# Performance work log

Hardware: AMD Instinct MI355X
Metric: run time of the kernel (lower is better)

## Reference

```python
import jax, jax.numpy as jnp
import numpy as np

VOXEL_SIZE = 0.4
GAMMA = 1.1  # VoxelPointsSampler.GAMMA
PC_MIN, PC_MAX = -75.2, 75.2


def setup_inputs() -> dict:
    key = jax.random.key(0)
    ks = jax.random.split(key, 6)
    N, M, C, S = 200000, 256, 5, 128
    xy = jax.random.uniform(ks[0], (N, 2), minval=PC_MIN, maxval=PC_MAX)
    z = jax.random.uniform(ks[1], (N, 1), minval=-2.0, maxval=4.0)
    feat = jax.random.normal(ks[2], (N, C - 3))
    points = jnp.concatenate([xy, z, feat], axis=1)  # [N, 5]
    ctr = jax.random.uniform(ks[3], (M, 2), minval=PC_MIN * 0.9, maxval=PC_MAX * 0.9)
    cz = jnp.zeros((M, 1), jnp.float32)
    dims = jax.random.uniform(ks[4], (M, 3), minval=1.0, maxval=5.0)
    yaw = jax.random.uniform(ks[5], (M, 1), minval=-3.14, maxval=3.14)
    boxes = jnp.concatenate([ctr, cz, dims, yaw], axis=1)  # [M, 7]
    pc_start = jnp.array([PC_MIN, PC_MIN], dtype=jnp.float32)
    return {"points": points, "boxes": boxes, "pc_start": pc_start, "num_sample": S}


def reference(points, boxes, pc_start, num_sample):
    N, C = points.shape
    M = boxes.shape[0]
    # --- voxel-level radius ball query (distances in voxel units) ---
    pcoords = (points[:, :2] - pc_start) / VOXEL_SIZE          # [N, 2]
    qcoords = (boxes[:, :2] - pc_start) / VOXEL_SIZE           # [M, 2]
    r_vox = jnp.linalg.norm(boxes[:, 3:5] * 0.5, axis=-1) * GAMMA / VOXEL_SIZE  # [M]
    dist = jnp.linalg.norm(qcoords[:, None, :] - pcoords[None, :, :], axis=-1)  # [M, N]
    vmask = (dist < r_vox[:, None]).any(axis=0)                # [N]
    # --- cylindrical pool (metric space); invalid points pushed out of every radius ---
    BIG = jnp.asarray(1e6, points.dtype)
    xy_m = jnp.where(vmask[:, None], points[:, :2], BIG)       # [N, 2]
    radii = jnp.linalg.norm(boxes[:, 3:5] * 0.5, axis=-1) * GAMMA  # [M]
    dis = jnp.linalg.norm(boxes[:, None, :2] - xy_m[None, :, :], axis=-1)  # [M, N]
    pmask = (dis <= radii[:, None]).astype(points.dtype)       # 0/1 [M, N]
    sm, sidx = jax.lax.top_k(pmask, num_sample)                # [M, S]
    smb = sm > 0.5                                             # bool [M, S]
    # unique indices across all sampled slots (fixed-size for jit)
    uniq, inv = jnp.unique(sidx.ravel(), return_inverse=True,
                           size=M * num_sample, fill_value=0)
    query_points = points[uniq]                                # [M*S, C] (padded)
    sampled_points = points[sidx] * smb[:, :, None]            # [M, S, C]
    idx = inv.reshape(M, num_sample).astype(jnp.int32) * smb   # [M, S]
    return sampled_points, idx, query_points
```

## Files before the change

### kernel.cpp

```cpp
#include <hip/hip_runtime.h>

typedef unsigned long long u64;
typedef unsigned int u32;
typedef unsigned short u16;
typedef unsigned char u8;

#define VOX 0.4f
#define GAM 1.1f
#define NCX 16
#define CELLW 32.0f
#define CAP 64

__device__ __forceinline__ float dist2d(float ax, float ay, float bx, float by) {
  float dx = __fsub_rn(ax, bx);
  float dy = __fsub_rn(ay, by);
  return __fsqrt_rn(__fadd_rn(__fmul_rn(dx, dx), __fmul_rn(dy, dy)));
}

__device__ __forceinline__ float box_radius(const float* __restrict__ boxes, int m) {
  float hx = __fmul_rn(boxes[m * 7 + 3], 0.5f);
  float hy = __fmul_rn(boxes[m * 7 + 4], 0.5f);
  float nr = __fsqrt_rn(__fadd_rn(__fmul_rn(hx, hx), __fmul_rn(hy, hy)));
  return __fmul_rn(nr, GAM);
}

__device__ __forceinline__ void box_voxel(const float* __restrict__ boxes, int m,
                                          float psx, float psy,
                                          float& qx, float& qy, float& r) {
  qx = __fdiv_rn(__fsub_rn(boxes[m * 7 + 0], psx), VOX);
  qy = __fdiv_rn(__fsub_rn(boxes[m * 7 + 1], psy), VOX);
  float hx = __fmul_rn(boxes[m * 7 + 3], 0.5f);
  float hy = __fmul_rn(boxes[m * 7 + 4], 0.5f);
  float nr = __fsqrt_rn(__fadd_rn(__fmul_rn(hx, hx), __fmul_rn(hy, hy)));
  r = __fdiv_rn(__fmul_rn(nr, GAM), VOX);
}

__global__ void k_prep(const float* __restrict__ boxes, const float* __restrict__ pc_start,
                       float* __restrict__ qxv, float* __restrict__ qyv, float* __restrict__ rv,
                       int* __restrict__ cellCnt, u16* __restrict__ cellList, int M) {
  const int tid = threadIdx.x;
  if (blockIdx.x == 0) {
    for (int m = tid; m < M; m += 256) {
      float qx, qy, r;
      box_voxel(boxes, m, pc_start[0], pc_start[1], qx, qy, r);
      qxv[m] = qx; qyv[m] = qy; rv[m] = r;
    }
    return;
  }
  const int cell = blockIdx.x - 1;
  const int cx = cell & (NCX - 1), cy = cell >> 4;
  const int wv = tid >> 6, lane = tid & 63;
  __shared__ int wcnt[4];
  const float x0 = (cx == 0) ? -3e38f : cx * CELLW;
  const float x1 = (cx == NCX - 1) ? 3e38f : (cx + 1) * CELLW;
  const float y0 = (cy == 0) ? -3e38f : cy * CELLW;
  const float y1 = (cy == NCX - 1) ? 3e38f : (cy + 1) * CELLW;
  bool hit = false;
  if (tid < M) {
    float qx, qy, r;
    box_voxel(boxes, tid, pc_start[0], pc_start[1], qx, qy, r);
    float ddx = fmaxf(0.0f, fmaxf(x0 - qx, qx - x1));
    float ddy = fmaxf(0.0f, fmaxf(y0 - qy, qy - y1));
    float rr = r + 0.01f;
    hit = (ddx * ddx + ddy * ddy <= rr * rr);
  }
  u64 b = __ballot(hit);
  if (lane == 0) wcnt[wv] = __popcll(b);
  __syncthreads();
  int base = 0;
  for (int w = 0; w < wv; ++w) base += wcnt[w];
  if (hit) {
    int slot = base + __popcll(b & ((1ULL << lane) - 1ULL));
    if (slot < CAP) cellList[cell * CAP + slot] = (u16)tid;
  }
  if (tid == 0) cellCnt[cell] = wcnt[0] + wcnt[1] + wcnt[2] + wcnt[3];
}

__global__ void k_vmask_count(const float* __restrict__ pts, const float* __restrict__ boxes,
                              const float* __restrict__ qxv, const float* __restrict__ qyv,
                              const float* __restrict__ rv,
                              const int* __restrict__ cellCnt, const u16* __restrict__ cellList,
                              u64* __restrict__ vbits, u64* __restrict__ pbits,
                              u64* __restrict__ bmG, int* __restrict__ cpng,
                              const float* __restrict__ pc_start,
                              int N, int M) {
  __shared__ float cpx[256], cpy[256];
  __shared__ int cpn[256];
  __shared__ int ccell[256];
  __shared__ float sbx[256], sby[256], sbr[256];
  __shared__ u64 bm[256][4];
  __shared__ int wcnt[4];
  const int tid = threadIdx.x;
  const int blk = blockIdx.x;
  const int n = blk * 256 + tid;
  const int wv = tid >> 6, lane = tid & 63;
  const float psx = pc_start[0], psy = pc_start[1];
  const bool valid = (n < N);

  bm[tid][0] = 0; bm[tid][1] = 0; bm[tid][2] = 0; bm[tid][3] = 0;
  if (tid < 4) pbits[blk * 4 + tid] = 0;
  if (tid < M) {
    sbx[tid] = boxes[tid * 7 + 0];
    sby[tid] = boxes[tid * 7 + 1];
    sbr[tid] = box_radius(boxes, tid);
  }

  float px = 1e6f, py = 1e6f, pvx = 0.f, pvy = 0.f;
  if (valid) {
    px = pts[n * 5 + 0];
    py = pts[n * 5 + 1];
    pvx = __fdiv_rn(__fsub_rn(px, psx), VOX);
    pvy = __fdiv_rn(__fsub_rn(py, psy), VOX);
  }

  bool flag = false;
  int mycell = 0;
  if (valid) {
    int cx = (int)floorf(pvx * (1.0f / CELLW));
    int cy = (int)floorf(pvy * (1.0f / CELLW));
    cx = cx < 0 ? 0 : (cx > NCX - 1 ? NCX - 1 : cx);
    cy = cy < 0 ? 0 : (cy > NCX - 1 ? NCX - 1 : cy);
    mycell = cy * NCX + cx;
    const int k = cellCnt[mycell];
    if (k <= CAP) {
      for (int j = 0; j < k; ++j) {
        const int m = cellList[mycell * CAP + j];
        float d = dist2d(qxv[m], qyv[m], pvx, pvy);
        if (d < rv[m]) { flag = true; break; }
      }
    } else {
      for (int m = 0; m < M; ++m) {
        float d = dist2d(qxv[m], qyv[m], pvx, pvy);
        if (d < rv[m]) { flag = true; break; }
      }
    }
  }
  u64 b = __ballot(flag);
  if (lane == 0) {
    vbits[n >> 6] = b;
    wcnt[wv] = __popcll(b);
  }
  __syncthreads();

  int base = 0;
  for (int w = 0; w < wv; ++w) base += wcnt[w];
  if (flag) {
    int slot = base + __popcll(b & ((1ULL << lane) - 1ULL));
    cpx[slot] = px;
    cpy[slot] = py;
    cpn[slot] = n;
    ccell[slot] = mycell;
  }
  __syncthreads();
  const int nfl = wcnt[0] + wcnt[1] + wcnt[2] + wcnt[3];
  if (tid < nfl) cpng[blk * 256 + tid] = cpn[tid];

  if (tid < nfl) {
    const float mx = cpx[tid], my = cpy[tid];
    const int cell = ccell[tid];
    const int k = cellCnt[cell];
    const u64 bit = 1ULL << (tid & 63);
    const int word = tid >> 6;
    if (k <= CAP) {
      for (int j = 0; j < k; ++j) {
        const int m = cellList[cell * CAP + j];
        float d = dist2d(sbx[m], sby[m], mx, my);
        if (d <= sbr[m]) atomicOr(&bm[m][word], bit);
      }
    } else {
      for (int m = 0; m < M; ++m) {
        float d = dist2d(sbx[m], sby[m], mx, my);
        if (d <= sbr[m]) atomicOr(&bm[m][word], bit);
      }
    }
  }
  __syncthreads();

  if (tid < M) {
    u64* dst = bmG + ((size_t)blk * M + tid) * 4;
    dst[0] = bm[tid][0]; dst[1] = bm[tid][1];
    dst[2] = bm[tid][2]; dst[3] = bm[tid][3];
  }
}

__global__ void __launch_bounds__(1024) k_scanfill(
    const float* __restrict__ pts, const float* __restrict__ boxes,
    const u64* __restrict__ bmG, const int* __restrict__ cpng,
    const u64* __restrict__ vbits, int* __restrict__ kcount,
    int* __restrict__ sidx, u64* __restrict__ pbits,
    int N, int M, int S, int nchunk) {
  const int m = blockIdx.x;
  const int t = threadIdx.x;
  const int lane = t & 63, wv = t >> 6;
  __shared__ int wsum[16];
  __shared__ int zws[16];

  u64 w0 = 0, w1 = 0, w2 = 0, w3 = 0;
  int v = 0;
  if (t < nchunk) {
    const u64* bp = bmG + ((size_t)t * M + m) * 4;
    w0 = bp[0]; w1 = bp[1]; w2 = bp[2]; w3 = bp[3];
    v = __popcll(w0) + __popcll(w1) + __popcll(w2) + __popcll(w3);
  }
  int incl = v;
  for (int d = 1; d < 64; d <<= 1) {
    int x = __shfl_up(incl, d);
    if (lane >= d) incl += x;
  }
  if (lane == 63) wsum[wv] = incl;
  __syncthreads();
  if (t < 16) {
    int s = wsum[t];
    for (int d = 1; d < 16; d <<= 1) {
      int x = __shfl_up(s, d);
      if (t >= d) s += x;
    }
    wsum[t] = s;
  }
  __syncthreads();
  const int wbase = (wv > 0) ? wsum[wv - 1] : 0;
  const int off = wbase + incl - v;
  const int total = wsum[15];
  const int k0 = total < S ? total : S;
  if (t == 0) kcount[m] = k0;

  if (t < nchunk && v > 0 && off < S) {
    const int* pbase = cpng + t * 256;
    int cum = off;
    int curw = -1;
    u64 acc = 0;
    u64 ws4[4] = {w0, w1, w2, w3};
    for (int wi = 0; wi < 4 && cum < S; ++wi) {
      u64 w = ws4[wi];
      while (w && cum < S) {
        int j = (wi << 6) + __builtin_ctzll(w);
        w &= w - 1;
        int pn = pbase[j];
        sidx[m * S + cum] = pn;
        const int wd = pn >> 6;
        if (wd != curw) {
          if (curw >= 0) atomicOr(&pbits[curw], acc);
          curw = wd;
          acc = 0;
        }
        acc |= 1ULL << (pn & 63);
        ++cum;
      }
    }
    if (curw >= 0) atomicOr(&pbits[curw], acc);
  }

  if (k0 >= S) return;
  const float bx = boxes[m * 7 + 0], by = boxes[m * 7 + 1];
  const float r = box_radius(boxes, m);
  const u64 ltmask = (1ULL << lane) - 1ULL;
  int fill = k0;
  for (int p0 = 0; p0 < N && fill < S; p0 += 1024) {
    const int n = p0 + t;
    const bool validn = n < N;
    bool one = false;
    if (validn) {
      u64 wbit = vbits[n >> 6];
      if ((wbit >> (n & 63)) & 1ULL) {
        float d = dist2d(bx, by, pts[n * 5 + 0], pts[n * 5 + 1]);
        one = (d <= r);
      }
    }
    const bool z = validn && !one;
    u64 b = __ballot(z);
    if (lane == 0) zws[wv] = __popcll(b);
    __syncthreads();
    int zbase = 0, ztot = 0;
    for (int ww = 0; ww < 16; ++ww) {
      int c = zws[ww];
      if (ww < wv) zbase += c;
      ztot += c;
    }
    bool setp = false;
    if (z) {
      int pos = fill + zbase + __popcll(b & ltmask);
      if (pos < S) { sidx[m * S + pos] = n; setp = true; }
    }
    u64 setmask = __ballot(setp);
    if (lane == 0 && setmask) atomicOr(&pbits[n >> 6], setmask);
    fill += ztot;
    __syncthreads();
  }
}

__global__ void __launch_bounds__(1024) k_sumscan(const u64* __restrict__ pbits,
                                                  int* __restrict__ boff, int nb) {
  __shared__ int wsum[16];
  const int t = threadIdx.x, lane = t & 63, wv = t >> 6;
  int v = 0;
  if (t < nb) {
    const u64* p = pbits + (size_t)t * 4;
    v = __popcll(p[0]) + __popcll(p[1]) + __popcll(p[2]) + __popcll(p[3]);
  }
  int incl = v;
  for (int d = 1; d < 64; d <<= 1) {
    int x = __shfl_up(incl, d);
    if (lane >= d) incl += x;
  }
  if (lane == 63) wsum[wv] = incl;
  __syncthreads();
  if (t < 16) {
    int s = wsum[t];
    for (int d = 1; d < 16; d <<= 1) {
      int x = __shfl_up(s, d);
      if (t >= d) s += x;
    }
    wsum[t] = s;
  }
  __syncthreads();
  const int base = (wv > 0) ? wsum[wv - 1] : 0;
  if (t < nb) boff[t] = base + incl - v;
  if (t == 0) boff[1024] = wsum[15];
}

__global__ void k_outpad(const float* __restrict__ pts, const int* __restrict__ sidx,
                         const int* __restrict__ kcount, const u64* __restrict__ pbits,
                         const int* __restrict__ boff,
                         float* __restrict__ out_samp, float* __restrict__ out_idx,
                         float* __restrict__ out_query, int MS, int S) {
  const int e = blockIdx.x * 256 + threadIdx.x;
  if (e >= MS) return;
  const int U = boff[1024];
  if (e >= U) {
    float* q = out_query + (size_t)e * 5;
    q[0] = pts[0]; q[1] = pts[1]; q[2] = pts[2]; q[3] = pts[3]; q[4] = pts[4];
  }
  const int m = e / S;
  const int s = e - m * S;
  const int n = sidx[e];
  const int c = n >> 8, w = n >> 6;
  int rank = boff[c];
  for (int k = c * 4; k < w; ++k) rank += __popcll(pbits[k]);
  rank += __popcll(pbits[w] & ((1ULL << (n & 63)) - 1ULL));
  const float* p = pts + (size_t)n * 5;
  float* q = out_query + (size_t)rank * 5;
  q[0] = p[0]; q[1] = p[1]; q[2] = p[2]; q[3] = p[3]; q[4] = p[4];
  float* o = out_samp + (size_t)e * 5;
  if (s < kcount[m]) {
    o[0] = p[0]; o[1] = p[1]; o[2] = p[2]; o[3] = p[3]; o[4] = p[4];
    out_idx[e] = (float)rank;
  } else {
    o[0] = 0.f; o[1] = 0.f; o[2] = 0.f; o[3] = 0.f; o[4] = 0.f;
    out_idx[e] = 0.f;
  }
}

extern "C" void kernel_launch(void* const* d_in, const int* in_sizes, int n_in,
                              void* d_out, int out_size, void* d_ws, size_t ws_size,
                              hipStream_t stream) {
  const float* pts = (const float*)d_in[0];
  const float* boxes = (const float*)d_in[1];
  const float* pc_start = (const float*)d_in[2];
  const int N = in_sizes[0] / 5;
  const int M = in_sizes[1] / 7;
  const int S = out_size / (M * 11);
  const int MS = M * S;

  float* out_samp = (float*)d_out;
  float* out_idx = out_samp + (size_t)MS * 5;
  float* out_query = out_idx + (size_t)MS;

  const int nb = (N + 255) / 256;
  const int nchunk = nb;

  char* w = (char*)d_ws;
  auto take = [&](size_t bytes) {
    char* p = w;
    w += (bytes + 15) & ~(size_t)15;
    return (void*)p;
  };
  u64* vbits     = (u64*)take((size_t)(nb * 4) * 8);
  u64* pbits     = (u64*)take((size_t)(nb * 4) * 8);
  u64* bmG       = (u64*)take((size_t)nchunk * M * 4 * 8);
  int* cpng      = (int*)take((size_t)nchunk * 256 * 4);
  int* sidx      = (int*)take((size_t)MS * 4);
  int* kcount    = (int*)take((size_t)M * 4);
  int* boff      = (int*)take((size_t)1025 * 4);
  float* qxv     = (float*)take((size_t)M * 4);
  float* qyv     = (float*)take((size_t)M * 4);
  float* rv      = (float*)take((size_t)M * 4);
  int* cellCnt   = (int*)take((size_t)NCX * NCX * 4);
  u16* cellList  = (u16*)take((size_t)NCX * NCX * CAP * 2);

  k_prep<<<NCX * NCX + 1, 256, 0, stream>>>(boxes, pc_start, qxv, qyv, rv,
                                            cellCnt, cellList, M);
  k_vmask_count<<<nb, 256, 0, stream>>>(pts, boxes, qxv, qyv, rv, cellCnt, cellList,
                                        vbits, pbits, bmG, cpng, pc_start, N, M);
  k_scanfill<<<M, 1024, 0, stream>>>(pts, boxes, bmG, cpng, vbits, kcount,
                                     sidx, pbits, N, M, S, nchunk);
  k_sumscan<<<1, 1024, 0, stream>>>(pbits, boff, nb);
  k_outpad<<<(MS + 255) / 256, 256, 0, stream>>>(pts, sidx, kcount, pbits, boff,
                                                 out_samp, out_idx, out_query, MS, S);
}
```

Before: 88.89 us.

## Fuse prefix-scan into output kernel and compute box voxel params in shared memory

Removes the single-block scan kernel: every block of the output kernel now recomputes the per-chunk prefix offsets of the selected-point bitmasks in shared memory, and launches with 1024 threads. Box voxel coordinates and radii, previously written to global memory by a dedicated block in the prep kernel, are now computed per block into shared memory inside the vmask kernel, with an added barrier. This saves one kernel launch and its global round trip, at the cost of redundant scan and box work in every block.

```diff
diff --git a/kernel.cpp b/kernel.cpp
--- a/kernel.cpp
+++ b/kernel.cpp
@@ -36,19 +36,10 @@
 }
 
 __global__ void k_prep(const float* __restrict__ boxes, const float* __restrict__ pc_start,
-                       float* __restrict__ qxv, float* __restrict__ qyv, float* __restrict__ rv,
                        int* __restrict__ cellCnt, u16* __restrict__ cellList, int M) {
+  const int cell = blockIdx.x;
+  const int cx = cell & (NCX - 1), cy = cell >> 4;
   const int tid = threadIdx.x;
-  if (blockIdx.x == 0) {
-    for (int m = tid; m < M; m += 256) {
-      float qx, qy, r;
-      box_voxel(boxes, m, pc_start[0], pc_start[1], qx, qy, r);
-      qxv[m] = qx; qyv[m] = qy; rv[m] = r;
-    }
-    return;
-  }
-  const int cell = blockIdx.x - 1;
-  const int cx = cell & (NCX - 1), cy = cell >> 4;
   const int wv = tid >> 6, lane = tid & 63;
   __shared__ int wcnt[4];
   const float x0 = (cx == 0) ? -3e38f : cx * CELLW;
@@ -77,8 +68,6 @@
 }
 
 __global__ void k_vmask_count(const float* __restrict__ pts, const float* __restrict__ boxes,
-                              const float* __restrict__ qxv, const float* __restrict__ qyv,
-                              const float* __restrict__ rv,
                               const int* __restrict__ cellCnt, const u16* __restrict__ cellList,
                               u64* __restrict__ vbits, u64* __restrict__ pbits,
                               u64* __restrict__ bmG, int* __restrict__ cpng,
@@ -88,6 +77,7 @@
   __shared__ int cpn[256];
   __shared__ int ccell[256];
   __shared__ float sbx[256], sby[256], sbr[256];
+  __shared__ float sqx[256], sqy[256], srv[256];
   __shared__ u64 bm[256][4];
   __shared__ int wcnt[4];
   const int tid = threadIdx.x;
@@ -103,6 +93,9 @@
     sbx[tid] = boxes[tid * 7 + 0];
     sby[tid] = boxes[tid * 7 + 1];
     sbr[tid] = box_radius(boxes, tid);
+    float qx, qy, r;
+    box_voxel(boxes, tid, psx, psy, qx, qy, r);
+    sqx[tid] = qx; sqy[tid] = qy; srv[tid] = r;
   }
 
   float px = 1e6f, py = 1e6f, pvx = 0.f, pvy = 0.f;
@@ -112,6 +105,7 @@
     pvx = __fdiv_rn(__fsub_rn(px, psx), VOX);
     pvy = __fdiv_rn(__fsub_rn(py, psy), VOX);
   }
+  __syncthreads();
 
   bool flag = false;
   int mycell = 0;
@@ -125,13 +119,13 @@
     if (k <= CAP) {
       for (int j = 0; j < k; ++j) {
         const int m = cellList[mycell * CAP + j];
-        float d = dist2d(qxv[m], qyv[m], pvx, pvy);
-        if (d < rv[m]) { flag = true; break; }
+        float d = dist2d(sqx[m], sqy[m], pvx, pvy);
+        if (d < srv[m]) { flag = true; break; }
       }
     } else {
       for (int m = 0; m < M; ++m) {
-        float d = dist2d(qxv[m], qyv[m], pvx, pvy);
-        if (d < rv[m]) { flag = true; break; }
+        float d = dist2d(sqx[m], sqy[m], pvx, pvy);
+        if (d < srv[m]) { flag = true; break; }
       }
     }
   }
@@ -288,12 +282,17 @@
   }
 }
 
-__global__ void __launch_bounds__(1024) k_sumscan(const u64* __restrict__ pbits,
-                                                  int* __restrict__ boff, int nb) {
+__global__ void __launch_bounds__(1024) k_outpad(
+    const float* __restrict__ pts, const int* __restrict__ sidx,
+    const int* __restrict__ kcount, const u64* __restrict__ pbits,
+    float* __restrict__ out_samp, float* __restrict__ out_idx,
+    float* __restrict__ out_query, int MS, int S, int nchunk) {
+  __shared__ int shb[1024];
   __shared__ int wsum[16];
   const int t = threadIdx.x, lane = t & 63, wv = t >> 6;
+
   int v = 0;
-  if (t < nb) {
+  if (t < nchunk) {
     const u64* p = pbits + (size_t)t * 4;
     v = __popcll(p[0]) + __popcll(p[1]) + __popcll(p[2]) + __popcll(p[3]);
   }
@@ -313,19 +312,12 @@
     wsum[t] = s;
   }
   __syncthreads();
-  const int base = (wv > 0) ? wsum[wv - 1] : 0;
-  if (t < nb) boff[t] = base + incl - v;
-  if (t == 0) boff[1024] = wsum[15];
-}
-
-__global__ void k_outpad(const float* __restrict__ pts, const int* __restrict__ sidx,
-                         const int* __restrict__ kcount, const u64* __restrict__ pbits,
-                         const int* __restrict__ boff,
-                         float* __restrict__ out_samp, float* __restrict__ out_idx,
-                         float* __restrict__ out_query, int MS, int S) {
-  const int e = blockIdx.x * 256 + threadIdx.x;
+  shb[t] = ((wv > 0) ? wsum[wv - 1] : 0) + incl - v;
+  const int U = wsum[15];
+  __syncthreads();
+
+  const int e = blockIdx.x * 1024 + t;
   if (e >= MS) return;
-  const int U = boff[1024];
   if (e >= U) {
     float* q = out_query + (size_t)e * 5;
     q[0] = pts[0]; q[1] = pts[1]; q[2] = pts[2]; q[3] = pts[3]; q[4] = pts[4];
@@ -334,7 +326,7 @@
   const int s = e - m * S;
   const int n = sidx[e];
   const int c = n >> 8, w = n >> 6;
-  int rank = boff[c];
+  int rank = shb[c];
   for (int k = c * 4; k < w; ++k) rank += __popcll(pbits[k]);
   rank += __popcll(pbits[w] & ((1ULL << (n & 63)) - 1ULL));
   const float* p = pts + (size_t)n * 5;
@@ -380,20 +372,15 @@
   int* cpng      = (int*)take((size_t)nchunk * 256 * 4);
   int* sidx      = (int*)take((size_t)MS * 4);
   int* kcount    = (int*)take((size_t)M * 4);
-  int* boff      = (int*)take((size_t)1025 * 4);
-  float* qxv     = (float*)take((size_t)M * 4);
-  float* qyv     = (float*)take((size_t)M * 4);
-  float* rv      = (float*)take((size_t)M * 4);
   int* cellCnt   = (int*)take((size_t)NCX * NCX * 4);
   u16* cellList  = (u16*)take((size_t)NCX * NCX * CAP * 2);
 
-  k_prep<<<NCX * NCX + 1, 256, 0, stream>>>(boxes, pc_start, qxv, qyv, rv,
-                                            cellCnt, cellList, M);
-  k_vmask_count<<<nb, 256, 0, stream>>>(pts, boxes, qxv, qyv, rv, cellCnt, cellList,
+  k_prep<<<NCX * NCX, 256, 0, stream>>>(boxes, pc_start, cellCnt, cellList, M);
+  k_vmask_count<<<nb, 256, 0, stream>>>(pts, boxes, cellCnt, cellList,
                                         vbits, pbits, bmG, cpng, pc_start, N, M);
   k_scanfill<<<M, 1024, 0, stream>>>(pts, boxes, bmG, cpng, vbits, kcount,
                                      sidx, pbits, N, M, S, nchunk);
-  k_sumscan<<<1, 1024, 0, stream>>>(pbits, boff, nb);
-  k_outpad<<<(MS + 255) / 256, 256, 0, stream>>>(pts, sidx, kcount, pbits, boff,
-                                                 out_samp, out_idx, out_query, MS, S);
-}
+  k_outpad<<<(MS + 1023) / 1024, 1024, 0, stream>>>(pts, sidx, kcount, pbits,
+                                                    out_samp, out_idx, out_query,
+                                                    MS, S, nchunk);
+}
```

Measured after the change: 87.86 us. Within noise of the previous version (-1.2%).
